# Kernel tuning notes

Hardware: AMD Instinct MI355X
Metric: run time of the kernel (lower is better)

Reference implementation:

```python
import jax, jax.numpy as jnp
import numpy as np

B, DX, DY = 128, 3, 3
D = DX * DY          # max_digit = 9
N = D * D            # num_nodes = 81
HID = 96
EMB = 16
ITERS = 4
M = B * N * D        # LSTM flattened rows = 93312


def _sudoku_adj():
    idx = np.arange(N)
    r, c = idx // D, idx % D
    br, bc = r // DX, c // DY
    same = (r[:, None] == r[None]) | (c[:, None] == c[None]) | ((br[:, None] == br[None]) & (bc[:, None] == bc[None]))
    return (same & ~np.eye(N, dtype=bool)).astype(np.float32)


def setup_inputs() -> dict:
    key = jax.random.key(0)
    ks = iter(jax.random.split(key, 40))

    def dense(shape, fan_in):
        return jax.random.normal(next(ks), shape, jnp.float32) / np.float32(np.sqrt(fan_in))

    return {
        "inputs": jax.random.randint(next(ks), (B, N), 0, D + 1, jnp.int32),
        "c0": jax.random.normal(next(ks), (M, HID), jnp.float32),
        "adj_cell": jnp.asarray((np.ones((D, D)) - np.eye(D)).astype(np.float32)),
        "adj_digit": jnp.asarray(_sudoku_adj()),
        "enc_W1": dense((3, EMB), 3), "enc_b1": jnp.zeros((EMB,), jnp.float32),
        "enc_W2": dense((EMB, HID), EMB), "enc_b2": jnp.zeros((HID,), jnp.float32),
        "cr_W": dense((3, HID, HID), HID), "cr_b": jnp.zeros((3, HID), jnp.float32),
        "dr_W": dense((3, HID, HID), HID), "dr_b": jnp.zeros((3, HID), jnp.float32),
        "gm_W1": dense((3 * HID, HID), 3 * HID), "gm_b1": jnp.zeros((HID,), jnp.float32),
        "gm_W2": dense((2, HID, HID), HID), "gm_b2": jnp.zeros((2, HID), jnp.float32),
        "lstm_Wih": dense((4 * HID, HID), HID), "lstm_Whh": dense((4 * HID, HID), HID),
        "lstm_bih": jnp.zeros((4 * HID,), jnp.float32), "lstm_bhh": jnp.zeros((4 * HID,), jnp.float32),
        "r_W12": dense((2, HID, HID), HID), "r_b12": jnp.zeros((2, HID), jnp.float32),
        "r_W3": dense((HID, 1), HID), "r_b3": jnp.zeros((1,), jnp.float32),
        "iters": ITERS,
    }


def _mlp(x, Ws, bs):
    # stacked MLP: ReLU between layers, none after the last
    L = Ws.shape[0]
    for l in range(L):
        x = x @ Ws[l] + bs[l]
        if l < L - 1:
            x = jax.nn.relu(x)
    return x


def _forward(inputs, c0, adj_cell, adj_digit, enc_W1, enc_b1, enc_W2, enc_b2,
             cr_W, cr_b, dr_W, dr_b, gm_W1, gm_b1, gm_W2, gm_b2,
             lstm_Wih, lstm_Whh, lstm_bih, lstm_bhh, r_W12, r_b12, r_W3, r_b3, iters):
    # mask: [B,N,D,3] = (blank, equals digit d+1, filled-with-other-digit)
    eq = inputs[:, :, None] == jnp.arange(1, D + 1, dtype=inputs.dtype)[None, None, :]
    given = inputs != 0
    mask = jnp.stack([
        jnp.broadcast_to((~given)[:, :, None], eq.shape), eq,
        (~eq) & given[:, :, None]
    ], axis=-1).astype(jnp.float32)

    X = jax.nn.relu(mask @ enc_W1 + enc_b1) @ enc_W2 + enc_b2  # [B,N,D,HID]

    def lstm_step(x, h, c):
        gates = x @ lstm_Wih.T + lstm_bih + h @ lstm_Whh.T + lstm_bhh
        i, f, g, o = jnp.split(gates, 4, axis=-1)  # PyTorch gate order i,f,g,o
        c = jax.nn.sigmoid(f) * c + jax.nn.sigmoid(i) * jnp.tanh(g)
        h = jax.nn.sigmoid(o) * jnp.tanh(c)
        return h, c

    def step(carry, _):
        h, c = carry  # [M,HID] each
        Hn = h.reshape(X.shape)
        # relational message passing: per-node MLP then sum over graph edges
        msg_cell = jnp.einsum('bndh,de->bneh', _mlp(Hn, cr_W, cr_b), adj_cell)
        msg_digit = jnp.einsum('bndh,nm->bmdh', _mlp(Hn, dr_W, dr_b), adj_digit)
        g = jnp.concatenate([X, msg_cell, msg_digit], axis=-1)  # [B,N,D,3*HID]
        g = jax.nn.relu(g @ gm_W1 + gm_b1)
        g = jax.nn.relu(g @ gm_W2[0] + gm_b2[0])
        g = g @ gm_W2[1] + gm_b2[1]
        h, c = lstm_step(g.reshape(-1, HID), h, c)
        Hn = h.reshape(X.shape)
        out = jax.nn.relu(Hn @ r_W12[0] + r_b12[0])
        out = jax.nn.relu(out @ r_W12[1] + r_b12[1])
        out = (out @ r_W3 + r_b3)[..., 0]  # [B,N,D]
        return (h, c), out

    (_, _), outs = jax.lax.scan(step, (X.reshape(-1, HID), c0), None, length=iters)
    return outs  # [iters,B,N,D]


def reference(inputs, c0, adj_cell, adj_digit, enc_W1, enc_b1, enc_W2, enc_b2,
              cr_W, cr_b, dr_W, dr_b, gm_W1, gm_b1, gm_W2, gm_b2,
              lstm_Wih, lstm_Whh, lstm_bih, lstm_bhh, r_W12, r_b12, r_W3, r_b3, iters):
    return _forward(inputs, c0, adj_cell, adj_digit, enc_W1, enc_b1, enc_W2, enc_b2,
                    cr_W, cr_b, dr_W, dr_b, gm_W1, gm_b1, gm_W2, gm_b2,
                    lstm_Wih, lstm_Whh, lstm_bih, lstm_bhh, r_W12, r_b12, r_W3, r_b3, iters)
```

## Files before the change

### kernel.cpp

```cpp
#include <hip/hip_runtime.h>
#include <hip/hip_bf16.h>

typedef unsigned short u16;
typedef __bf16 bf16x8 __attribute__((ext_vector_type(8)));
typedef float  f32x4  __attribute__((ext_vector_type(4)));
typedef u16    u16x8  __attribute__((ext_vector_type(8)));

#define HID   96
#define LDP   104
#define MROWS 93312
#define BN    10368
#define GRID_TILE 1458
#define FUSE_GRID 5832
#define SGX   100
#define PST   97

#define FCH 9216

#define MFMA(a,b,c) __builtin_amdgcn_mfma_f32_16x16x32_bf16((a),(b),(c),0,0,0)

__device__ __forceinline__ float bf2f(u16 x){
  union { float f; unsigned u; } v; v.u = ((unsigned)x) << 16; return v.f;
}
__device__ __forceinline__ u16 f2bf(float f){
  union { float f; unsigned u; } v; v.f = f;
  unsigned r = v.u + 0x7fffu + ((v.u >> 16) & 1u);
  return (u16)(r >> 16);
}
__device__ __forceinline__ float frcp(float x){ return __builtin_amdgcn_rcpf(x); }
__device__ __forceinline__ float sigf(float x){ return frcp(1.f + __expf(-x)); }
__device__ __forceinline__ float tanhf_(float x){
  float xx = fminf(fmaxf(x, -15.f), 15.f);
  float e = __expf(-2.f * xx);
  return (1.f - e) * frcp(1.f + e);
}
__device__ __forceinline__ void lds_fence(){
  asm volatile("s_waitcnt lgkmcnt(0)" ::: "memory");
}

struct Frags { bf16x8 a0, a1, a2; };

__device__ __forceinline__ Frags load_afrags_g(const u16* __restrict__ A, size_t row0, int lane){
  int t16 = lane & 15, q = lane >> 4;
  const u16* p = A + (row0 + (size_t)t16) * 96 + q * 8;
  Frags f;
  f.a0 = *reinterpret_cast<const bf16x8*>(p);
  f.a1 = *reinterpret_cast<const bf16x8*>(p + 32);
  f.a2 = *reinterpret_cast<const bf16x8*>(p + 64);
  return f;
}
__device__ __forceinline__ Frags load_afrags_s(const u16* sA, int row0, int lane){
  int t16 = lane & 15, q = lane >> 4;
  const u16* p = sA + (row0 + t16) * LDP + q * 8;
  Frags f;
  f.a0 = *reinterpret_cast<const bf16x8*>(p);
  f.a1 = *reinterpret_cast<const bf16x8*>(p + 32);
  f.a2 = *reinterpret_cast<const bf16x8*>(p + 64);
  return f;
}

__device__ __forceinline__ void layer_g(Frags f, const u16* __restrict__ wb,
    const float* __restrict__ bias, u16* dst, int dstStride, size_t rowBase,
    bool relu, int lane)
{
  int t16 = lane & 15, q = lane >> 4;
  #pragma unroll
  for (int nt = 0; nt < 6; nt++){
    float b = bias ? bias[nt * 16 + t16] : 0.f;
    f32x4 acc = {b, b, b, b};
    const u16* wp = wb + nt * 1536 + lane * 8;
    acc = MFMA(f.a0, *reinterpret_cast<const bf16x8*>(wp),        acc);
    acc = MFMA(f.a1, *reinterpret_cast<const bf16x8*>(wp + 512),  acc);
    acc = MFMA(f.a2, *reinterpret_cast<const bf16x8*>(wp + 1024), acc);
    #pragma unroll
    for (int j = 0; j < 4; j++){
      float v = acc[j];
      if (relu) v = fmaxf(v, 0.f);
      dst[(rowBase + q * 4 + j) * (size_t)dstStride + nt * 16 + t16] = f2bf(v);
    }
  }
}

__device__ __forceinline__ void layer_split(Frags f, const u16* __restrict__ wb,
    const float* __restrict__ bias, u16* dst, bool relu, int lane, int w)
{
  int t16 = lane & 15, q = lane >> 4;
  #pragma unroll
  for (int nt = w; nt < 6; nt += 4){
    float b = bias ? bias[nt * 16 + t16] : 0.f;
    f32x4 acc = {b, b, b, b};
    const u16* wp = wb + nt * 1536 + lane * 8;
    acc = MFMA(f.a0, *reinterpret_cast<const bf16x8*>(wp),        acc);
    acc = MFMA(f.a1, *reinterpret_cast<const bf16x8*>(wp + 512),  acc);
    acc = MFMA(f.a2, *reinterpret_cast<const bf16x8*>(wp + 1024), acc);
    #pragma unroll
    for (int j = 0; j < 4; j++){
      float v = acc[j];
      if (relu) v = fmaxf(v, 0.f);
      dst[(q * 4 + j) * LDP + nt * 16 + t16] = f2bf(v);
    }
  }
}

__device__ __forceinline__ void layer_split_gout(Frags f, const u16* __restrict__ wb,
    const float* __restrict__ bias, u16* gdst, size_t rbase, bool relu, int lane, int w)
{
  int t16 = lane & 15, q = lane >> 4;
  #pragma unroll
  for (int nt = w; nt < 6; nt += 4){
    float b = bias ? bias[nt * 16 + t16] : 0.f;
    f32x4 acc = {b, b, b, b};
    const u16* wp = wb + nt * 1536 + lane * 8;
    acc = MFMA(f.a0, *reinterpret_cast<const bf16x8*>(wp),        acc);
    acc = MFMA(f.a1, *reinterpret_cast<const bf16x8*>(wp + 512),  acc);
    acc = MFMA(f.a2, *reinterpret_cast<const bf16x8*>(wp + 1024), acc);
    #pragma unroll
    for (int j = 0; j < 4; j++){
      float v = acc[j];
      if (relu) v = fmaxf(v, 0.f);
      gdst[(rbase + q * 4 + j) * 96 + nt * 16 + t16] = f2bf(v);
    }
  }
}

__device__ __forceinline__ void mfma6_g(f32x4* acc, Frags f,
    const u16* __restrict__ wb, int lane)
{
  #pragma unroll
  for (int jt = 0; jt < 6; jt++){
    const u16* wp = wb + jt * 1536 + lane * 8;
    acc[jt] = MFMA(f.a0, *reinterpret_cast<const bf16x8*>(wp),        acc[jt]);
    acc[jt] = MFMA(f.a1, *reinterpret_cast<const bf16x8*>(wp + 512),  acc[jt]);
    acc[jt] = MFMA(f.a2, *reinterpret_cast<const bf16x8*>(wp + 1024), acc[jt]);
  }
}

__global__ __launch_bounds__(256) void k_prep2(const float* __restrict__ crW,
    const float* __restrict__ drW, const float* __restrict__ gmW2,
    const float* __restrict__ rW12, const float* __restrict__ Whh,
    u16* __restrict__ pWB)
{
  int b = blockIdx.x, tid = threadIdx.x;
  if (b < 7){
    const float* src; int ch;
    if      (b == 0){ src = crW;          ch = 0;  }
    else if (b == 1){ src = crW  + 9216;  ch = 1;  }
    else if (b == 2){ src = drW;          ch = 3;  }
    else if (b == 3){ src = drW  + 9216;  ch = 4;  }
    else if (b == 4){ src = gmW2;         ch = 8;  }
    else if (b == 5){ src = rW12;         ch = 10; }
    else            { src = rW12 + 9216;  ch = 11; }
    u16* dst = pWB + ch * FCH;
    #pragma unroll
    for (int i = 0; i < 36; i++){
      int idx = tid + i * 256;
      int f = idx >> 9, rem = idx & 511, l = rem >> 3, j = rem & 7;
      int nt = f / 3, kc = f - nt * 3;
      int n = nt * 16 + (l & 15);
      int k = ((l >> 4) << 3) + kc * 32 + j;
      dst[idx] = f2bf(src[k * 96 + n]);
    }
  } else {
    int bb = b - 7;
    u16* dst = pWB + (16 + bb) * FCH;
    const float* src = Whh + bb * 9216;
    #pragma unroll
    for (int i = 0; i < 36; i++){
      int idx = tid + i * 256;
      int f = idx >> 9, rem = idx & 511, l = rem >> 3, j = rem & 7;
      int nt = f / 3, kc = f - nt * 3;
      int n = nt * 16 + (l & 15);
      int k = ((l >> 4) << 3) + kc * 32 + j;
      dst[idx] = f2bf(src[n * 96 + k]);
    }
  }
}

__global__ __launch_bounds__(256) void k_prepc(const float* __restrict__ crW,
    const float* __restrict__ crB, const float* __restrict__ drW,
    const float* __restrict__ drB, const float* __restrict__ gmW1,
    u16* __restrict__ pWB, float* __restrict__ bY, float* __restrict__ bZ)
{
  __shared__ float sM[96 * PST];
  __shared__ float sW[96 * PST];
  int b = blockIdx.x, g = b / 9, seg = b - g * 9, tid = threadIdx.x;
  const float* L = (g == 0 ? crW : drW) + 2 * 9216;
  const float* R = gmW1 + (g == 0 ? 9216 : 18432);
  for (int i = tid; i < 9216; i += 256){
    int r = i / 96, cc = i - r * 96;
    sM[r * PST + cc] = L[i];
    sW[r * PST + cc] = R[i];
  }
  __syncthreads();
  if (seg == 0){
    const float* bv = (g == 0 ? crB : drB) + 192;
    float* bo = (g == 0 ? bY : bZ);
    for (int n = tid; n < 96; n += 256){
      float a = 0.f;
      for (int j = 0; j < 96; j++) a += bv[j] * sW[j * PST + n];
      bo[n] = a;
    }
  }
  u16* dst = pWB + (g == 0 ? 2 : 5) * FCH;
  #pragma unroll
  for (int i = 0; i < 4; i++){
    int idx = seg * 1024 + tid + i * 256;
    int f = idx >> 9, rem = idx & 511, l = rem >> 3, j = rem & 7;
    int nt = f / 3, kc = f - nt * 3;
    int n = nt * 16 + (l & 15);
    int k = ((l >> 4) << 3) + kc * 32 + j;
    float a = 0.f;
    #pragma unroll 4
    for (int jj = 0; jj < 96; jj++) a += sM[k * PST + jj] * sW[jj * PST + n];
    dst[idx] = f2bf(a);
  }
}

__global__ __launch_bounds__(256) void k_prepf(const float* __restrict__ gmW2,
    const float* __restrict__ Wih, u16* __restrict__ pWB)
{
  __shared__ float sW[96 * PST];
  int b = blockIdx.x, g = b / 9, seg = b - g * 9, tid = threadIdx.x;
  for (int i = tid; i < 9216; i += 256){
    int r = i / 96, cc = i - r * 96;
    sW[r * PST + cc] = gmW2[9216 + i];
  }
  __syncthreads();
  u16* dst = pWB + (12 + g) * FCH;
  #pragma unroll
  for (int i = 0; i < 4; i++){
    int idx = seg * 1024 + tid + i * 256;
    int f = idx >> 9, rem = idx & 511, l = rem >> 3, j = rem & 7;
    int nt = f / 3, kc = f - nt * 3;
    int n = nt * 16 + (l & 15);
    int k = ((l >> 4) << 3) + kc * 32 + j;
    const float* wr = Wih + (g * 96 + n) * 96;
    float a = 0.f;
    #pragma unroll 4
    for (int jj = 0; jj < 96; jj++) a += sW[k * PST + jj] * wr[jj];
    dst[idx] = f2bf(a);
  }
}

__global__ void k_tables(const float* __restrict__ eW1, const float* __restrict__ eb1,
                         const float* __restrict__ eW2, const float* __restrict__ eb2,
                         const float* __restrict__ gmW1, const float* __restrict__ gmb1,
                         const float* __restrict__ bih, const float* __restrict__ bhh,
                         const float* __restrict__ gmb2, const float* __restrict__ Wih,
                         float* __restrict__ XTab, float* __restrict__ XgTab,
                         float* __restrict__ bsx)
{
  __shared__ float sX[3][96];
  int j = threadIdx.x;
  for (int n = j; n < 384; n += 128){
    float acc = bih[n] + bhh[n];
    const float* wr = Wih + n * 96;
    for (int jj = 0; jj < 96; jj++) acc += gmb2[96 + jj] * wr[jj];
    bsx[n] = acc;
  }
  if (j < 96){
    for (int ch = 0; ch < 3; ch++){
      float acc = eb2[j];
      for (int e = 0; e < 16; e++){
        float hv = fmaxf(eW1[ch * 16 + e] + eb1[e], 0.f);
        acc += hv * eW2[e * 96 + j];
      }
      sX[ch][j] = acc;
      XTab[ch * 96 + j] = acc;
    }
  }
  __syncthreads();
  if (j < 96){
    for (int ch = 0; ch < 3; ch++){
      float acc = gmb1[j];
      for (int k = 0; k < 96; k++) acc += sX[ch][k] * gmW1[k * 96 + j];
      XgTab[ch * 96 + j] = acc;
    }
  }
}

__global__ __launch_bounds__(256) void k_init(const int* __restrict__ inputs,
    const float* __restrict__ XTab, u16* __restrict__ h)
{
  int idx = blockIdx.x * 256 + threadIdx.x;
  int m = idx / 12, h8 = idx - m * 12;
  int bn = m / 9, d = m - bn * 9;
  int inp = inputs[bn];
  int ch = (inp == 0) ? 0 : ((inp == d + 1) ? 1 : 2);
  const float* xt = XTab + ch * 96 + h8 * 8;
  u16* hp = h + (size_t)m * 96 + h8 * 8;
  #pragma unroll
  for (int e = 0; e < 8; e++) hp[e] = f2bf(xt[e]);
}

__global__ __launch_bounds__(256) void k_ab3(const u16* __restrict__ h,
    u16* __restrict__ Y, u16* __restrict__ Z,
    const u16* __restrict__ pWB, const float* __restrict__ crB,
    const float* __restrict__ drB, const float* __restrict__ bY,
    const float* __restrict__ bZ)
{
  __shared__ u16 sA[64 * LDP];
  const int tid = threadIdx.x, lane = tid & 63, wave = tid >> 6;
  const int wrow = wave * 16;
  const size_t rbase = (size_t)blockIdx.x * 64;

  Frags hf = load_afrags_g(h, rbase + wrow, lane);

  layer_g(hf, pWB, crB, sA, LDP, wrow, true, lane);                  lds_fence();
  Frags f = load_afrags_s(sA, wrow, lane);
  layer_g(f, pWB + 1 * FCH, crB + 96, sA, LDP, wrow, true, lane);    lds_fence();
  f = load_afrags_s(sA, wrow, lane);
  layer_g(f, pWB + 2 * FCH, bY, Y, 96, rbase + wrow, false, lane);
  lds_fence();

  layer_g(hf, pWB + 3 * FCH, drB, sA, LDP, wrow, true, lane);        lds_fence();
  f = load_afrags_s(sA, wrow, lane);
  layer_g(f, pWB + 4 * FCH, drB + 96, sA, LDP, wrow, true, lane);    lds_fence();
  f = load_afrags_s(sA, wrow, lane);
  layer_g(f, pWB + 5 * FCH, bZ, Z, 96, rbase + wrow, false, lane);
}

__device__ __forceinline__ void addrow(float* s, const u16* p){
  u16x8 t = *reinterpret_cast<const u16x8*>(p);
  #pragma unroll
  for (int e = 0; e < 8; e++) s[e] += bf2f(t[e]);
}

__global__ __launch_bounds__(256) void k_msg(u16* __restrict__ Z,
    const u16* __restrict__ Y, u16* __restrict__ Ssum)
{
  __shared__ u16 sT[81 * LDP];
  const int tid = threadIdx.x;
  if (blockIdx.x >= 1152){
    int idx = (blockIdx.x - 1152) * 256 + tid;
    int bn = idx / 12, h8 = idx - bn * 12;
    const u16* base = Y + (size_t)bn * 864 + h8 * 8;
    float s[8];
    #pragma unroll
    for (int e = 0; e < 8; e++) s[e] = 0.f;
    #pragma unroll
    for (int d = 0; d < 9; d++){
      u16x8 v = *reinterpret_cast<const u16x8*>(base + d * 96);
      #pragma unroll
      for (int e = 0; e < 8; e++) s[e] += bf2f(v[e]);
    }
    u16x8 o;
    #pragma unroll
    for (int e = 0; e < 8; e++) o[e] = f2bf(s[e]);
    *reinterpret_cast<u16x8*>(Ssum + (size_t)bn * 96 + h8 * 8) = o;
    return;
  }
  const int b = blockIdx.x / 9, d = blockIdx.x - b * 9;
  const size_t base = ((size_t)b * 729 + d) * 96;
  for (int i = tid; i < 972; i += 256){
    int n = i / 12, k8 = i - n * 12;
    *reinterpret_cast<u16x8*>(sT + n * LDP + k8 * 8) =
      *reinterpret_cast<const u16x8*>(Z + base + (size_t)n * 864 + k8 * 8);
  }
  __syncthreads();
  for (int i = tid; i < 972; i += 256){
    int m = i / 12, k8 = i - m * 12;
    int r = m / 9, cc = m - r * 9;
    int br = (r / 3) * 3, bc = (cc / 3) * 3;
    float s[8];
    #pragma unroll
    for (int e = 0; e < 8; e++) s[e] = 0.f;
    #pragma unroll
    for (int c2 = 0; c2 < 9; c2++) if (c2 != cc) addrow(s, sT + (r * 9 + c2) * LDP + k8 * 8);
    #pragma unroll
    for (int r2 = 0; r2 < 9; r2++) if (r2 != r) addrow(s, sT + (r2 * 9 + cc) * LDP + k8 * 8);
    #pragma unroll
    for (int r2 = 0; r2 < 3; r2++)
      #pragma unroll
      for (int c2 = 0; c2 < 3; c2++){
        int rr = br + r2, c3 = bc + c2;
        if (rr != r && c3 != cc) addrow(s, sT + (rr * 9 + c3) * LDP + k8 * 8);
      }
    u16x8 o;
    #pragma unroll
    for (int e = 0; e < 8; e++) o[e] = f2bf(s[e]);
    *reinterpret_cast<u16x8*>(Z + base + (size_t)m * 864 + k8 * 8) = o;
  }
}

__global__ __launch_bounds__(256, 4) void k_fuse16x(u16* Y, u16* Z,
    const u16* __restrict__ Ssum,
    const int* __restrict__ inputs, const float* __restrict__ XgTab,
    const u16* __restrict__ pWB, const float* __restrict__ gmb2,
    u16* h, const float* cin, float* cout,
    const float* __restrict__ bsx, const float* __restrict__ rb12,
    const float* __restrict__ rW3, const float* __restrict__ rb3,
    float* __restrict__ out, const float* __restrict__ crB,
    const float* __restrict__ drB, const float* __restrict__ bY,
    const float* __restrict__ bZ, int doAB)
{
  __shared__ u16 sA[16 * LDP];
  __shared__ u16 sB[16 * LDP];
  __shared__ float sG[4][16][SGX];
  u16* sC = reinterpret_cast<u16*>(sG);
  const int tid = threadIdx.x, lane = tid & 63, w = tid >> 6;
  const int t16 = lane & 15, q = lane >> 4;
  const size_t rbase = (size_t)blockIdx.x * 16;

  float cpre[6];
  #pragma unroll
  for (int e = 0; e < 6; e++){
    int idx = e * 256 + tid;
    int r = idx / 96, col = idx - r * 96;
    cpre[e] = cin[(rbase + r) * 96 + col];
  }
  Frags fh = load_afrags_g(h, rbase, lane);

  if (tid < 192){
    int rl = tid / 12, kc = tid - rl * 12;
    int m = (int)rbase + rl;
    int bn = m / 9, d = m - bn * 9;
    int inp = inputs[bn];
    int ch = (inp == 0) ? 0 : ((inp == d + 1) ? 1 : 2);
    const float* xg = XgTab + ch * 96 + kc * 8;
    u16x8 vy = *reinterpret_cast<const u16x8*>(Y    + (size_t)m * 96 + kc * 8);
    u16x8 vz = *reinterpret_cast<const u16x8*>(Z    + (size_t)m * 96 + kc * 8);
    u16x8 vs = *reinterpret_cast<const u16x8*>(Ssum + (size_t)bn * 96 + kc * 8);
    u16x8 o;
    #pragma unroll
    for (int e = 0; e < 8; e++)
      o[e] = f2bf(fmaxf(xg[e] + bf2f(vs[e]) - bf2f(vy[e]) + bf2f(vz[e]), 0.f));
    *reinterpret_cast<u16x8*>(sA + rl * LDP + kc * 8) = o;
  }
  __syncthreads();

  {
    Frags f = load_afrags_s(sA, 0, lane);
    layer_split(f, pWB + 8 * FCH, gmb2, sB, true, lane, w);
  }
  __syncthreads();

  f32x4 acc[6];
  #pragma unroll
  for (int nt = 0; nt < 6; nt++){
    float b = bsx[w * 96 + nt * 16 + t16];
    f32x4 a = {b, b, b, b};
    acc[nt] = a;
  }
  {
    Frags fa = load_afrags_s(sB, 0, lane);
    mfma6_g(acc, fa, pWB + (12 + w) * FCH, lane);
    mfma6_g(acc, fh, pWB + (16 + w) * FCH, lane);
  }
  #pragma unroll
  for (int nt = 0; nt < 6; nt++)
    #pragma unroll
    for (int j = 0; j < 4; j++)
      sG[w][q * 4 + j][nt * 16 + t16] = acc[nt][j];
  __syncthreads();

  #pragma unroll
  for (int e = 0; e < 6; e++){
    int idx = e * 256 + tid;
    int r = idx / 96, col = idx - r * 96;
    float iv = sG[0][r][col];
    float fv = sG[1][r][col];
    float gv = sG[2][r][col];
    float ov = sG[3][r][col];
    size_t m = rbase + r;
    float cn = sigf(fv) * cpre[e] + sigf(iv) * tanhf_(gv);
    float hn = sigf(ov) * tanhf_(cn);
    cout[m * 96 + col] = cn;
    u16 hb = f2bf(hn);
    h[m * 96 + col] = hb;
    sA[r * LDP + col] = hb;
  }
  __syncthreads();

  {
    Frags f = load_afrags_s(sA, 0, lane);
    layer_split(f, pWB + 10 * FCH, rb12, sB, true, lane, w);
  }
  __syncthreads();
  {
    Frags f = load_afrags_s(sB, 0, lane);
    layer_split(f, pWB + 11 * FCH, rb12 + 96, sC, true, lane, w);
  }
  __syncthreads();

  if (tid < 64){
    int row = tid >> 2, part = tid & 3;
    float s = 0.f;
    const u16* rp = sC + row * LDP + part * 24;
    #pragma unroll
    for (int k = 0; k < 24; k++) s += bf2f(rp[k]) * rW3[part * 24 + k];
    s += __shfl_xor(s, 1);
    s += __shfl_xor(s, 2);
    if (part == 0) out[rbase + row] = s + rb3[0];
  }
  if (doAB){
    {
      Frags f = load_afrags_s(sA, 0, lane);
      layer_split(f, pWB + 0 * FCH, crB, sB, true, lane, w);
    }
    __syncthreads();
    {
      Frags f = load_afrags_s(sB, 0, lane);
      layer_split(f, pWB + 1 * FCH, crB + 96, sC, true, lane, w);
    }
    __syncthreads();
    {
      Frags f = load_afrags_s(sC, 0, lane);
      layer_split_gout(f, pWB + 2 * FCH, bY, Y, rbase, false, lane, w);
      Frags f2 = load_afrags_s(sA, 0, lane);
      layer_split(f2, pWB + 3 * FCH, drB, sB, true, lane, w);
    }
    __syncthreads();
    {
      Frags f = load_afrags_s(sB, 0, lane);
      layer_split(f, pWB + 4 * FCH, drB + 96, sC, true, lane, w);
    }
    __syncthreads();
    {
      Frags f = load_afrags_s(sC, 0, lane);
      layer_split_gout(f, pWB + 5 * FCH, bZ, Z, rbase, false, lane, w);
    }
  }
}

extern "C" void kernel_launch(void* const* d_in, const int* in_sizes, int n_in,
                              void* d_out, int out_size, void* d_ws, size_t ws_size,
                              hipStream_t stream)
{
  (void)in_sizes; (void)n_in; (void)out_size; (void)ws_size;
  const int*   inputs = (const int*)d_in[0];
  const float* c0     = (const float*)d_in[1];
  const float* eW1  = (const float*)d_in[4];
  const float* eb1  = (const float*)d_in[5];
  const float* eW2  = (const float*)d_in[6];
  const float* eb2  = (const float*)d_in[7];
  const float* crW  = (const float*)d_in[8];
  const float* crB  = (const float*)d_in[9];
  const float* drW  = (const float*)d_in[10];
  const float* drB  = (const float*)d_in[11];
  const float* gmW1 = (const float*)d_in[12];
  const float* gmb1 = (const float*)d_in[13];
  const float* gmW2 = (const float*)d_in[14];
  const float* gmb2 = (const float*)d_in[15];
  const float* Wih  = (const float*)d_in[16];
  const float* Whh  = (const float*)d_in[17];
  const float* bih  = (const float*)d_in[18];
  const float* bhh  = (const float*)d_in[19];
  const float* rW12 = (const float*)d_in[20];
  const float* rb12 = (const float*)d_in[21];
  const float* rW3  = (const float*)d_in[22];
  const float* rb3  = (const float*)d_in[23];

  char* ws = (char*)d_ws;
  float* XgTab = (float*)(ws);
  float* XTab  = (float*)(ws + 4096);
  float* bsx   = (float*)(ws + 6144);
  float* bY    = (float*)(ws + 7680);
  float* bZ    = (float*)(ws + 8064);
  u16*   pWB   = (u16*)(ws + 8704);
  u16* h  = (u16*)(ws + 409600);
  u16* B1 = h  + (size_t)MROWS * 96;
  u16* B2 = B1 + (size_t)MROWS * 96;
  float* c = (float*)(B2 + (size_t)MROWS * 96);
  u16* Ssum = (u16*)(c + (size_t)MROWS * 96);
  float* out = (float*)d_out;

  k_prep2<<<11, 256, 0, stream>>>(crW, drW, gmW2, rW12, Whh, pWB);
  k_prepc<<<18, 256, 0, stream>>>(crW, crB, drW, drB, gmW1, pWB, bY, bZ);
  k_prepf<<<36, 256, 0, stream>>>(gmW2, Wih, pWB);
  k_tables<<<1, 128, 0, stream>>>(eW1, eb1, eW2, eb2, gmW1, gmb1, bih, bhh,
                                  gmb2, Wih, XTab, XgTab, bsx);
  k_init<<<(MROWS * 12) / 256, 256, 0, stream>>>(inputs, XTab, h);
  k_ab3<<<GRID_TILE, 256, 0, stream>>>(h, B1, B2, pWB, crB, drB, bY, bZ);

  for (int it = 0; it < 4; ++it){
    const float* cin = (it == 0) ? c0 : c;
    k_msg<<<1152 + 486, 256, 0, stream>>>(B2, B1, Ssum);
    k_fuse16x<<<FUSE_GRID, 256, 0, stream>>>(B1, B2, Ssum, inputs, XgTab, pWB,
                                             gmb2, h, cin, c, bsx, rb12, rW3, rb3,
                                             out + (size_t)it * MROWS,
                                             crB, drB, bY, bZ, (it < 3) ? 1 : 0);
  }
}
```

Baseline: 661.0 us.

## Compute sudoku digit message aggregation as MFMA adjacency matmul; halve LSTM gate LDS staging

The scalar neighbour-sum loop in k_msg becomes a bf16 MFMA product of a precomputed 96x96 padded sudoku adjacency matrix with the staged Z tile. Z is rearranged in LDS into B-fragment layout. Separately, k_fuse16x stages the LSTM gate accumulators through a half-size LDS buffer in two passes, which cuts LDS use to improve occupancy but adds extra barriers. The MFMA path does some padded wasted work and changes the accumulation order.

```diff
diff --git a/kernel.cpp b/kernel.cpp
--- a/kernel.cpp
+++ b/kernel.cpp
@@ -176,6 +176,22 @@
   }
 }
 
+__global__ __launch_bounds__(256) void k_prepadj(u16* __restrict__ adjM)
+{
+  int tid = threadIdx.x;
+  for (int i = tid; i < 9216; i += 256){
+    int m = i / 96, n = i - (i / 96) * 96;
+    float v = 0.f;
+    if (m < 81 && n < 81 && m != n){
+      int rm = m / 9, cm = m - rm * 9;
+      int rn = n / 9, cn = n - rn * 9;
+      if (rm == rn || cm == cn || ((rm / 3 == rn / 3) && (cm / 3 == cn / 3)))
+        v = 1.f;
+    }
+    adjM[i] = f2bf(v);
+  }
+}
+
 __global__ __launch_bounds__(256) void k_prepc(const float* __restrict__ crW,
     const float* __restrict__ crB, const float* __restrict__ drW,
     const float* __restrict__ drB, const float* __restrict__ gmW1,
@@ -320,16 +336,11 @@
   layer_g(f, pWB + 5 * FCH, bZ, Z, 96, rbase + wrow, false, lane);
 }
 
-__device__ __forceinline__ void addrow(float* s, const u16* p){
-  u16x8 t = *reinterpret_cast<const u16x8*>(p);
-  #pragma unroll
-  for (int e = 0; e < 8; e++) s[e] += bf2f(t[e]);
-}
-
 __global__ __launch_bounds__(256) void k_msg(u16* __restrict__ Z,
-    const u16* __restrict__ Y, u16* __restrict__ Ssum)
-{
-  __shared__ u16 sT[81 * LDP];
+    const u16* __restrict__ Y, u16* __restrict__ Ssum,
+    const u16* __restrict__ adjM)
+{
+  __shared__ u16 sF[9216];
   const int tid = threadIdx.x;
   if (blockIdx.x >= 1152){
     int idx = (blockIdx.x - 1152) * 256 + tid;
@@ -352,34 +363,39 @@
   }
   const int b = blockIdx.x / 9, d = blockIdx.x - b * 9;
   const size_t base = ((size_t)b * 729 + d) * 96;
-  for (int i = tid; i < 972; i += 256){
-    int n = i / 12, k8 = i - n * 12;
-    *reinterpret_cast<u16x8*>(sT + n * LDP + k8 * 8) =
-      *reinterpret_cast<const u16x8*>(Z + base + (size_t)n * 864 + k8 * 8);
-  }
-  __syncthreads();
-  for (int i = tid; i < 972; i += 256){
-    int m = i / 12, k8 = i - m * 12;
-    int r = m / 9, cc = m - r * 9;
-    int br = (r / 3) * 3, bc = (cc / 3) * 3;
-    float s[8];
-    #pragma unroll
-    for (int e = 0; e < 8; e++) s[e] = 0.f;
-    #pragma unroll
-    for (int c2 = 0; c2 < 9; c2++) if (c2 != cc) addrow(s, sT + (r * 9 + c2) * LDP + k8 * 8);
-    #pragma unroll
-    for (int r2 = 0; r2 < 9; r2++) if (r2 != r) addrow(s, sT + (r2 * 9 + cc) * LDP + k8 * 8);
-    #pragma unroll
-    for (int r2 = 0; r2 < 3; r2++)
-      #pragma unroll
-      for (int c2 = 0; c2 < 3; c2++){
-        int rr = br + r2, c3 = bc + c2;
-        if (rr != r && c3 != cc) addrow(s, sT + (rr * 9 + c3) * LDP + k8 * 8);
-      }
-    u16x8 o;
-    #pragma unroll
-    for (int e = 0; e < 8; e++) o[e] = f2bf(s[e]);
-    *reinterpret_cast<u16x8*>(Z + base + (size_t)m * 864 + k8 * 8) = o;
+  for (int i = tid; i < 1152; i += 256){
+    int n = i / 12, k8 = i - (i / 12) * 12;
+    u16x8 v;
+    if (n < 81){
+      v = *reinterpret_cast<const u16x8*>(Z + base + (size_t)n * 864 + k8 * 8);
+    } else {
+      for (int e = 0; e < 8; e++) v[e] = 0;
+    }
+    int f = (k8 >> 1) * 3 + (n >> 5);
+    int lbase = ((n >> 3) & 3) * 16 + (k8 & 1) * 8;
+    u16* p = sF + f * 512 + lbase * 8 + (n & 7);
+    #pragma unroll
+    for (int e = 0; e < 8; e++) p[e * 8] = v[e];
+  }
+  __syncthreads();
+  const int lane = tid & 63, w = tid >> 6;
+  const int t16 = lane & 15, q = lane >> 4;
+  #pragma unroll
+  for (int ti = 0; ti < 9; ti++){
+    int t = w + ti * 4;
+    int mt = t / 6, nt = t - mt * 6;
+    Frags fa = load_afrags_g(adjM, mt * 16, lane);
+    f32x4 acc = {0.f, 0.f, 0.f, 0.f};
+    const u16* bp = sF + nt * 1536 + lane * 8;
+    acc = MFMA(fa.a0, *reinterpret_cast<const bf16x8*>(bp),        acc);
+    acc = MFMA(fa.a1, *reinterpret_cast<const bf16x8*>(bp + 512),  acc);
+    acc = MFMA(fa.a2, *reinterpret_cast<const bf16x8*>(bp + 1024), acc);
+    int c = nt * 16 + t16;
+    #pragma unroll
+    for (int jr = 0; jr < 4; jr++){
+      int m = mt * 16 + q * 4 + jr;
+      if (m < 81) Z[base + (size_t)m * 864 + c] = f2bf(acc[jr]);
+    }
   }
 }
 
@@ -396,8 +412,8 @@
 {
   __shared__ u16 sA[16 * LDP];
   __shared__ u16 sB[16 * LDP];
-  __shared__ float sG[4][16][SGX];
-  u16* sC = reinterpret_cast<u16*>(sG);
+  __shared__ float sGh[4][8][SGX];
+  u16* sC = reinterpret_cast<u16*>(sGh);
   const int tid = threadIdx.x, lane = tid & 63, w = tid >> 6;
   const int t16 = lane & 15, q = lane >> 4;
   const size_t rbase = (size_t)blockIdx.x * 16;
@@ -447,23 +463,51 @@
     mfma6_g(acc, fa, pWB + (12 + w) * FCH, lane);
     mfma6_g(acc, fh, pWB + (16 + w) * FCH, lane);
   }
-  #pragma unroll
-  for (int nt = 0; nt < 6; nt++)
-    #pragma unroll
-    for (int j = 0; j < 4; j++)
-      sG[w][q * 4 + j][nt * 16 + t16] = acc[nt][j];
-  __syncthreads();
-
-  #pragma unroll
-  for (int e = 0; e < 6; e++){
+
+  if (q < 2){
+    #pragma unroll
+    for (int nt = 0; nt < 6; nt++)
+      #pragma unroll
+      for (int j = 0; j < 4; j++)
+        sGh[w][q * 4 + j][nt * 16 + t16] = acc[nt][j];
+  }
+  __syncthreads();
+  #pragma unroll
+  for (int e = 0; e < 3; e++){
     int idx = e * 256 + tid;
     int r = idx / 96, col = idx - r * 96;
-    float iv = sG[0][r][col];
-    float fv = sG[1][r][col];
-    float gv = sG[2][r][col];
-    float ov = sG[3][r][col];
+    float iv = sGh[0][r][col];
+    float fv = sGh[1][r][col];
+    float gv = sGh[2][r][col];
+    float ov = sGh[3][r][col];
     size_t m = rbase + r;
     float cn = sigf(fv) * cpre[e] + sigf(iv) * tanhf_(gv);
+    float hn = sigf(ov) * tanhf_(cn);
+    cout[m * 96 + col] = cn;
+    u16 hb = f2bf(hn);
+    h[m * 96 + col] = hb;
+    sA[r * LDP + col] = hb;
+  }
+  __syncthreads();
+
+  if (q >= 2){
+    #pragma unroll
+    for (int nt = 0; nt < 6; nt++)
+      #pragma unroll
+      for (int j = 0; j < 4; j++)
+        sGh[w][(q - 2) * 4 + j][nt * 16 + t16] = acc[nt][j];
+  }
+  __syncthreads();
+  #pragma unroll
+  for (int e = 0; e < 3; e++){
+    int idx = (e + 3) * 256 + tid;
+    int r = idx / 96, col = idx - r * 96;
+    float iv = sGh[0][r - 8][col];
+    float fv = sGh[1][r - 8][col];
+    float gv = sGh[2][r - 8][col];
+    float ov = sGh[3][r - 8][col];
+    size_t m = rbase + r;
+    float cn = sigf(fv) * cpre[e + 3] + sigf(iv) * tanhf_(gv);
     float hn = sigf(ov) * tanhf_(cn);
     cout[m * 96 + col] = cn;
     u16 hb = f2bf(hn);
@@ -563,11 +607,13 @@
   u16* B2 = B1 + (size_t)MROWS * 96;
   float* c = (float*)(B2 + (size_t)MROWS * 96);
   u16* Ssum = (u16*)(c + (size_t)MROWS * 96);
+  u16* adjM = Ssum + (size_t)BN * 96;
   float* out = (float*)d_out;
 
   k_prep2<<<11, 256, 0, stream>>>(crW, drW, gmW2, rW12, Whh, pWB);
   k_prepc<<<18, 256, 0, stream>>>(crW, crB, drW, drB, gmW1, pWB, bY, bZ);
   k_prepf<<<36, 256, 0, stream>>>(gmW2, Wih, pWB);
+  k_prepadj<<<1, 256, 0, stream>>>(adjM);
   k_tables<<<1, 128, 0, stream>>>(eW1, eb1, eW2, eb2, gmW1, gmb1, bih, bhh,
                                   gmb2, Wih, XTab, XgTab, bsx);
   k_init<<<(MROWS * 12) / 256, 256, 0, stream>>>(inputs, XTab, h);
@@ -575,7 +621,7 @@
 
   for (int it = 0; it < 4; ++it){
     const float* cin = (it == 0) ? c0 : c;
-    k_msg<<<1152 + 486, 256, 0, stream>>>(B2, B1, Ssum);
+    k_msg<<<1152 + 486, 256, 0, stream>>>(B2, B1, Ssum, adjM);
     k_fuse16x<<<FUSE_GRID, 256, 0, stream>>>(B1, B2, Ssum, inputs, XgTab, pWB,
                                              gmb2, h, cin, c, bsx, rb12, rW3, rb3,
                                              out + (size_t)it * MROWS,
```

After: 635.0 us. -3.9%, faster.
